# Performance work log

Hardware: AMD Instinct MI355X
Metric: run time of the kernel (lower is better)

Reference implementation:

```python
import jax, jax.numpy as jnp
import numpy as np

NUM_LAYERS = 2
N_NODES = 100000
N_EDGES = 1600000
D_FEAT = 48


def setup_inputs() -> dict:
    key = jax.random.key(0)
    k1, k2, k3 = jax.random.split(key, 3)
    features = jax.random.normal(k1, (N_NODES, D_FEAT), dtype=jnp.float32)
    edge_weight = jax.random.uniform(k2, (N_EDGES,), dtype=jnp.float32)
    edge_index = jax.random.randint(k3, (2, N_EDGES), 0, N_NODES, dtype=jnp.int64)
    return {"features": features, "edge_weight": edge_weight, "edge_index": edge_index}


def spmm(edge_index, edge_weight, x, n):
    # out[i] = sum_{e: dst[e]==i} w[e] * x[src[e]]  (LGConv with normalize=False)
    src, dst = edge_index[0], edge_index[1]
    msgs = x[src] * edge_weight[:, None]  # [E, d]
    return jax.ops.segment_sum(msgs, dst, num_segments=n)


def reference(features, edge_weight, edge_index):
    n = features.shape[0]
    scale = 1.0 / (NUM_LAYERS + 1)
    avg = features * scale
    x = features
    for _ in range(NUM_LAYERS):
        x = spmm(edge_index, edge_weight, x, n)
        avg = avg + x * scale
    return avg
```

## Files before the change

### kernel.cpp

```cpp
#include <hip/hip_runtime.h>
#include <hip/hip_fp16.h>


static constexpr int D = 48;
static constexpr int PD = 64;
static constexpr int CB = 256;
static constexpr int CSH = 8;
static constexpr int MAXNC = 512;
static constexpr int TILE = 4096;
static constexpr int TPB_A = 512;
static constexpr int EPT = TILE / TPB_A;
static constexpr int CAP = 4864;

__global__ void hc_tohalf(const float* __restrict__ in, __half* __restrict__ out,
                          int nchunk, int* __restrict__ gcur, int NC) {
    if (blockIdx.x == 0) {
        for (int i = threadIdx.x; i < NC; i += blockDim.x) gcur[i] = 0;
    }
    int i = blockIdx.x * blockDim.x + threadIdx.x;
    if (i >= nchunk) return;
    int node = i / 12, c = i % 12;
    float4 v = reinterpret_cast<const float4*>(in)[i];
    __half2* o = reinterpret_cast<__half2*>(out + (size_t)node * PD + c * 4);
    o[0] = __floats2half2_rn(v.x, v.y);
    o[1] = __floats2half2_rn(v.z, v.w);
}

__global__ __launch_bounds__(TPB_A) void hc_partA(const int* __restrict__ src,
                                                  const int* __restrict__ dst,
                                                  const float* __restrict__ w,
                                                  int* __restrict__ gcur,
                                                  int2* __restrict__ cw1,
                                                  int E, int NC) {
    __shared__ int2 stg[TILE];
    __shared__ unsigned short sbin[TILE];
    __shared__ int h[MAXNC], o[MAXNC], gb[MAXNC];
    __shared__ int sc[TPB_A];
    const int t = threadIdx.x;
    const int lo = blockIdx.x * TILE;
    const int cnt = min(TILE, E - lo);

    for (int i = t; i < NC; i += TPB_A) h[i] = 0;
    __syncthreads();

    int bn[EPT], rk[EPT];
    int2 val[EPT];
#pragma unroll
    for (int k = 0; k < EPT; ++k) {
        int idx = k * TPB_A + t;
        if (idx < cnt) {
            int e = lo + idx;
            int d = dst[e];
            int b = d >> CSH;
            bn[k] = b;
            rk[k] = atomicAdd(&h[b], 1);
            unsigned hw = __half_as_ushort(__float2half_rn(w[e]));
            val[k] = make_int2(src[e] | ((d & (CB - 1)) << 17),
                               (int)(hw | (hw << 16)));
        } else {
            bn[k] = -1;
        }
    }
    __syncthreads();

    int c0 = (t < NC) ? h[t] : 0;
    sc[t] = c0;
    __syncthreads();
    for (int off = 1; off < TPB_A; off <<= 1) {
        int u = (t >= off) ? sc[t - off] : 0;
        __syncthreads();
        sc[t] += u;
        __syncthreads();
    }
    if (t < NC) o[t] = sc[t] - c0;
    __syncthreads();

    for (int i = t; i < NC; i += TPB_A)
        gb[i] = h[i] ? (i * CAP + atomicAdd(&gcur[i], h[i])) : 0;
    __syncthreads();

#pragma unroll
    for (int k = 0; k < EPT; ++k) {
        if (bn[k] >= 0) {
            int slot = o[bn[k]] + rk[k];
            stg[slot] = val[k];
            sbin[slot] = (unsigned short)bn[k];
        }
    }
    __syncthreads();

    for (int i = t; i < cnt; i += TPB_A) {
        int b = sbin[i];
        cw1[gb[b] + i - o[b]] = stg[i];
    }
}

__global__ __launch_bounds__(512) void hc_scan_c(const int* __restrict__ gcur,
                                                 int* __restrict__ cstart, int NC) {
    __shared__ int sm[512];
    const int t = threadIdx.x;
    int v = (t < NC) ? gcur[t] : 0;
    sm[t] = v;
    __syncthreads();
    for (int off = 1; off < 512; off <<= 1) {
        int u = (t >= off) ? sm[t - off] : 0;
        __syncthreads();
        sm[t] += u;
        __syncthreads();
    }
    int excl = sm[t] - v;
    if (t < NC) cstart[t] = excl;
    if (t == NC) cstart[NC] = excl;
}

__global__ __launch_bounds__(512) void hc_partB(const int2* __restrict__ cw1,
                                                const int* __restrict__ gcur,
                                                const int* __restrict__ cstart,
                                                unsigned* __restrict__ cw2,
                                                int* __restrict__ row_ptr,
                                                int N) {
    __shared__ int cnt2[CB], st2[CB], cur2[CB];
    const int cb = blockIdx.x;
    const int t = threadIdx.x;
    const int rlo = cb * CAP;
    const int rcnt = gcur[cb];
    const int lo = cstart[cb];

    if (t < CB) cnt2[t] = 0;
    __syncthreads();
    for (int e = t; e < rcnt; e += 512)
        atomicAdd(&cnt2[(((unsigned)cw1[rlo + e].x) >> 17) & (CB - 1)], 1);
    __syncthreads();

    int v = (t < CB) ? cnt2[t] : 0;
    if (t < CB) st2[t] = v;
    __syncthreads();
    for (int off = 1; off < CB; off <<= 1) {
        int u = (t >= off && t < CB) ? st2[t - off] : 0;
        __syncthreads();
        if (t < CB) st2[t] += u;
        __syncthreads();
    }
    if (t < CB) {
        int excl = st2[t] - v;
        cur2[t] = excl;
        int node = cb * CB + t;
        if (node <= N) row_ptr[node] = lo + excl;
    }
    __syncthreads();

    for (int e = t; e < rcnt; e += 512) {
        int2 p = cw1[rlo + e];
        int dl = (((unsigned)p.x) >> 17) & (CB - 1);
        int pos = lo + atomicAdd(&cur2[dl], 1);
        unsigned srcn = (unsigned)p.x & 0x1FFFFu;
        unsigned w15 = ((unsigned)p.y & 0xFFFFu) >> 1;
        cw2[pos] = srcn | (w15 << 17);
    }
}

template <bool FINAL>
__global__ __launch_bounds__(256) void hc_gather(const __half* __restrict__ xin,
                                                 const int* __restrict__ row_ptr,
                                                 const unsigned* __restrict__ cw,
                                                 const __half* __restrict__ fh,
                                                 const __half* __restrict__ x1h,
                                                 void* __restrict__ outv, int N) {
    const int lane = threadIdx.x & 63;
    const int node = blockIdx.x * (blockDim.x >> 6) + (threadIdx.x >> 6);
    if (node >= N) return;
    const int eslot = lane >> 3;
    const int fl = lane & 7;

    const int start = row_ptr[node];
    const int end = row_ptr[node + 1];

    __half2 ac[3][3];
#pragma unroll
    for (int k = 0; k < 3; ++k)
#pragma unroll
        for (int j = 0; j < 3; ++j) ac[k][j] = __float2half2_rn(0.f);

#pragma unroll 1
    for (int eb = start; eb < end; eb += 24) {
#pragma unroll
        for (int k = 0; k < 3; ++k) {
            int e = eb + 8 * k + eslot;
            bool vld = e < end;
            int ec = vld ? e : end - 1;
            unsigned p = cw[ec];
            unsigned hw = (p >> 16) & 0xFFFEu;
            unsigned wb = vld ? (hw | (hw << 16)) : 0u;
            __half2 wh = *reinterpret_cast<const __half2*>(&wb);
            const uint3 u = *reinterpret_cast<const uint3*>(
                xin + (size_t)(p & 0x1FFFFu) * PD + fl * 6);
            ac[k][0] = __hfma2(*(const __half2*)&u.x, wh, ac[k][0]);
            ac[k][1] = __hfma2(*(const __half2*)&u.y, wh, ac[k][1]);
            ac[k][2] = __hfma2(*(const __half2*)&u.z, wh, ac[k][2]);
        }
    }

    float a[6];
#pragma unroll
    for (int j = 0; j < 3; ++j) {
        float2 s0 = __half22float2(ac[0][j]);
        float2 s1 = __half22float2(ac[1][j]);
        float2 s2 = __half22float2(ac[2][j]);
        float lo = s0.x + s1.x + s2.x;
        float hi = s0.y + s1.y + s2.y;
        lo += __shfl_xor(lo, 8);  hi += __shfl_xor(hi, 8);
        lo += __shfl_xor(lo, 16); hi += __shfl_xor(hi, 16);
        lo += __shfl_xor(lo, 32); hi += __shfl_xor(hi, 32);
        a[2 * j] = lo;
        a[2 * j + 1] = hi;
    }

    if (eslot == 0) {
        const long long bp = (long long)node * PD + fl * 6;
        if (FINAL) {
            float* out = (float*)outv;
            const long long bo = (long long)node * D + fl * 6;
            constexpr float s = 1.0f / 3.0f;
#pragma unroll
            for (int j = 0; j < 6; ++j)
                out[bo + j] =
                    (__half2float(fh[bp + j]) + __half2float(x1h[bp + j]) + a[j]) * s;
        } else {
            uint3 u;
            *(__half2*)&u.x = __floats2half2_rn(a[0], a[1]);
            *(__half2*)&u.y = __floats2half2_rn(a[2], a[3]);
            *(__half2*)&u.z = __floats2half2_rn(a[4], a[5]);
            *reinterpret_cast<uint3*>((__half*)outv + bp) = u;
        }
    }
}

extern "C" void kernel_launch(void* const* d_in, const int* in_sizes, int n_in,
                              void* d_out, int out_size, void* d_ws, size_t ws_size,
                              hipStream_t stream) {
    const float* features = (const float*)d_in[0];
    const float* ew       = (const float*)d_in[1];
    const int*   ei       = (const int*)d_in[2];

    const int E = in_sizes[1];
    const int N = in_sizes[0] / D;

    const int* src = ei;
    const int* dst = ei + E;

    const int NC = (N + CB - 1) / CB;
    const int NT = (E + TILE - 1) / TILE;

    char*     base   = (char*)d_ws;
    int2*     cw1    = (int2*)base;
    __half*   x1h    = (__half*)base;
    size_t    cw1_bytes = (size_t)NC * CAP * 8;
    unsigned* cw2    = (unsigned*)(base + cw1_bytes);
    __half*   fh     = (__half*)(cw2 + E);
    int*      row_ptr= (int*)(fh + (size_t)N * PD);
    int*      gcur   = row_ptr + (N + 1);
    int*      cstart = gcur + NC;

    const int nchunk = N * 12;
    hc_tohalf<<<(nchunk + 255) / 256, 256, 0, stream>>>(features, fh, nchunk,
                                                        gcur, NC);
    hc_partA<<<NT, TPB_A, 0, stream>>>(src, dst, ew, gcur, cw1, E, NC);
    hc_scan_c<<<1, 512, 0, stream>>>(gcur, cstart, NC);
    hc_partB<<<NC, 512, 0, stream>>>(cw1, gcur, cstart, cw2, row_ptr, N);

    const int ggrid = (N + 3) / 4;
    hc_gather<false><<<ggrid, 256, 0, stream>>>(fh, row_ptr, cw2,
                                                nullptr, nullptr, x1h, N);
    hc_gather<true><<<ggrid, 256, 0, stream>>>(x1h, row_ptr, cw2,
                                               fh, x1h, (float*)d_out, N);
}
```

Baseline: 115.4 us.

## Drop global bucket scan; use per-bucket row_ptr layout and wave-shuffle scans

Removes the single-block hc_scan_c kernel by giving each coarse bucket its own CAP-sized region in cw2 and a per-bucket row_ptr segment of CB+1 entries, so partB no longer needs global offsets. The block-level Hillis-Steele LDS scans in partA and partB are replaced with wave shuffle scans plus a small per-wave fixup, cutting barriers. Global bucket counters are padded by 16 ints to reduce atomic contention and false sharing. In exchange, cw2 grows to NC*CAP entries with gaps between buckets, and the gather computes a segmented row_ptr address.

Measured after the change: 110.5 us. 4.3% less time.

```diff
diff --git a/kernel.cpp b/kernel.cpp
--- a/kernel.cpp
+++ b/kernel.cpp
@@ -11,11 +11,12 @@
 static constexpr int TPB_A = 512;
 static constexpr int EPT = TILE / TPB_A;
 static constexpr int CAP = 4864;
+static constexpr int GPAD = 16;
 
 __global__ void hc_tohalf(const float* __restrict__ in, __half* __restrict__ out,
                           int nchunk, int* __restrict__ gcur, int NC) {
     if (blockIdx.x == 0) {
-        for (int i = threadIdx.x; i < NC; i += blockDim.x) gcur[i] = 0;
+        for (int i = threadIdx.x; i < NC * GPAD; i += blockDim.x) gcur[i] = 0;
     }
     int i = blockIdx.x * blockDim.x + threadIdx.x;
     if (i >= nchunk) return;
@@ -35,7 +36,7 @@
     __shared__ int2 stg[TILE];
     __shared__ unsigned short sbin[TILE];
     __shared__ int h[MAXNC], o[MAXNC], gb[MAXNC];
-    __shared__ int sc[TPB_A];
+    __shared__ int wsum[8];
     const int t = threadIdx.x;
     const int lo = blockIdx.x * TILE;
     const int cnt = min(TILE, E - lo);
@@ -64,19 +65,29 @@
     __syncthreads();
 
     int c0 = (t < NC) ? h[t] : 0;
-    sc[t] = c0;
-    __syncthreads();
-    for (int off = 1; off < TPB_A; off <<= 1) {
-        int u = (t >= off) ? sc[t - off] : 0;
-        __syncthreads();
-        sc[t] += u;
-        __syncthreads();
-    }
-    if (t < NC) o[t] = sc[t] - c0;
+    int incl = c0;
+#pragma unroll
+    for (int off = 1; off < 64; off <<= 1) {
+        int u = __shfl_up(incl, off);
+        if ((t & 63) >= off) incl += u;
+    }
+    if ((t & 63) == 63) wsum[t >> 6] = incl;
+    __syncthreads();
+    if (t == 0) {
+        int run = 0;
+#pragma unroll
+        for (int wv = 0; wv < 8; ++wv) {
+            int c = wsum[wv];
+            wsum[wv] = run;
+            run += c;
+        }
+    }
+    __syncthreads();
+    if (t < NC) o[t] = incl - c0 + wsum[t >> 6];
     __syncthreads();
 
     for (int i = t; i < NC; i += TPB_A)
-        gb[i] = h[i] ? (i * CAP + atomicAdd(&gcur[i], h[i])) : 0;
+        gb[i] = h[i] ? (i * CAP + atomicAdd(&gcur[i * GPAD], h[i])) : 0;
     __syncthreads();
 
 #pragma unroll
@@ -95,36 +106,18 @@
     }
 }
 
-__global__ __launch_bounds__(512) void hc_scan_c(const int* __restrict__ gcur,
-                                                 int* __restrict__ cstart, int NC) {
-    __shared__ int sm[512];
-    const int t = threadIdx.x;
-    int v = (t < NC) ? gcur[t] : 0;
-    sm[t] = v;
-    __syncthreads();
-    for (int off = 1; off < 512; off <<= 1) {
-        int u = (t >= off) ? sm[t - off] : 0;
-        __syncthreads();
-        sm[t] += u;
-        __syncthreads();
-    }
-    int excl = sm[t] - v;
-    if (t < NC) cstart[t] = excl;
-    if (t == NC) cstart[NC] = excl;
-}
-
 __global__ __launch_bounds__(512) void hc_partB(const int2* __restrict__ cw1,
                                                 const int* __restrict__ gcur,
-                                                const int* __restrict__ cstart,
                                                 unsigned* __restrict__ cw2,
                                                 int* __restrict__ row_ptr,
                                                 int N) {
-    __shared__ int cnt2[CB], st2[CB], cur2[CB];
+    __shared__ int cnt2[CB], cur2[CB];
+    __shared__ int wsum[4];
     const int cb = blockIdx.x;
     const int t = threadIdx.x;
     const int rlo = cb * CAP;
-    const int rcnt = gcur[cb];
-    const int lo = cstart[cb];
+    const int rcnt = gcur[cb * GPAD];
+    int* rp = row_ptr + cb * (CB + 1);
 
     if (t < CB) cnt2[t] = 0;
     __syncthreads();
@@ -133,26 +126,36 @@
     __syncthreads();
 
     int v = (t < CB) ? cnt2[t] : 0;
-    if (t < CB) st2[t] = v;
-    __syncthreads();
-    for (int off = 1; off < CB; off <<= 1) {
-        int u = (t >= off && t < CB) ? st2[t - off] : 0;
-        __syncthreads();
-        if (t < CB) st2[t] += u;
-        __syncthreads();
-    }
+    int incl = v;
+#pragma unroll
+    for (int off = 1; off < 64; off <<= 1) {
+        int u = __shfl_up(incl, off);
+        if ((t & 63) >= off) incl += u;
+    }
+    if ((t & 63) == 63 && (t >> 6) < 4) wsum[t >> 6] = incl;
+    __syncthreads();
+    if (t == 0) {
+        int run = 0;
+#pragma unroll
+        for (int wv = 0; wv < 4; ++wv) {
+            int c = wsum[wv];
+            wsum[wv] = run;
+            run += c;
+        }
+        rp[CB] = rlo + rcnt;
+    }
+    __syncthreads();
     if (t < CB) {
-        int excl = st2[t] - v;
+        int excl = incl - v + wsum[t >> 6];
         cur2[t] = excl;
-        int node = cb * CB + t;
-        if (node <= N) row_ptr[node] = lo + excl;
+        rp[t] = rlo + excl;
     }
     __syncthreads();
 
     for (int e = t; e < rcnt; e += 512) {
         int2 p = cw1[rlo + e];
         int dl = (((unsigned)p.x) >> 17) & (CB - 1);
-        int pos = lo + atomicAdd(&cur2[dl], 1);
+        int pos = rlo + atomicAdd(&cur2[dl], 1);
         unsigned srcn = (unsigned)p.x & 0x1FFFFu;
         unsigned w15 = ((unsigned)p.y & 0xFFFFu) >> 1;
         cw2[pos] = srcn | (w15 << 17);
@@ -172,8 +175,9 @@
     const int eslot = lane >> 3;
     const int fl = lane & 7;
 
-    const int start = row_ptr[node];
-    const int end = row_ptr[node + 1];
+    const int* rp = row_ptr + (node >> CSH) * (CB + 1) + (node & (CB - 1));
+    const int start = rp[0];
+    const int end = rp[1];
 
     __half2 ac[3][3];
 #pragma unroll
@@ -256,17 +260,15 @@
     __half*   x1h    = (__half*)base;
     size_t    cw1_bytes = (size_t)NC * CAP * 8;
     unsigned* cw2    = (unsigned*)(base + cw1_bytes);
-    __half*   fh     = (__half*)(cw2 + E);
+    __half*   fh     = (__half*)(cw2 + (size_t)NC * CAP);
     int*      row_ptr= (int*)(fh + (size_t)N * PD);
-    int*      gcur   = row_ptr + (N + 1);
-    int*      cstart = gcur + NC;
+    int*      gcur   = row_ptr + NC * (CB + 1);
 
     const int nchunk = N * 12;
     hc_tohalf<<<(nchunk + 255) / 256, 256, 0, stream>>>(features, fh, nchunk,
                                                         gcur, NC);
     hc_partA<<<NT, TPB_A, 0, stream>>>(src, dst, ew, gcur, cw1, E, NC);
-    hc_scan_c<<<1, 512, 0, stream>>>(gcur, cstart, NC);
-    hc_partB<<<NC, 512, 0, stream>>>(cw1, gcur, cstart, cw2, row_ptr, N);
+    hc_partB<<<NC, 512, 0, stream>>>(cw1, gcur, cw2, row_ptr, N);
 
     const int ggrid = (N + 3) / 4;
     hc_gather<false><<<ggrid, 256, 0, stream>>>(fh, row_ptr, cw2,
```
